# Performance work log

Measured on AMD Instinct MI355X. Metric: run time of the kernel, lower is better.

## Reference

```python
import jax, jax.numpy as jnp
import numpy as np

COMMITMENT_COST = 0.25
N, D, K = 131072, 64, 1024


def setup_inputs() -> dict:
    key = jax.random.key(0)
    k1, k2 = jax.random.split(key)
    inputs = jax.random.normal(k1, (N, D), dtype=jnp.float32)
    # torch init: uniform(-1/K, 1/K)
    weight = jax.random.uniform(k2, (K, D), dtype=jnp.float32,
                                minval=-1.0 / K, maxval=1.0 / K)
    return {"inputs": inputs, "weight": weight}


def reference(inputs, weight):
    x2 = jnp.sum(inputs * inputs, axis=1, keepdims=True)          # [N, 1]
    e2 = jnp.sum(weight * weight, axis=1)                          # [K]
    distances = x2 + e2 - 2.0 * jnp.matmul(inputs, weight.T)       # [N, K]
    encoding_indices = jnp.argmin(distances, axis=1)               # [N]
    # scatter one-hot + matmul in the original == direct gather
    quantized = jnp.take(weight, encoding_indices, axis=0)         # [N, D]
    e_latent_loss = jnp.mean((jax.lax.stop_gradient(quantized) - inputs) ** 2)
    q_latent_loss = jnp.mean((quantized - jax.lax.stop_gradient(inputs)) ** 2)
    loss = q_latent_loss + COMMITMENT_COST * e_latent_loss
    # straight-through estimator
    quantized_st = inputs + jax.lax.stop_gradient(quantized - inputs)
    return (quantized_st, loss, encoding_indices)
```

## Files before the change

kernel.cpp:

```cpp
#include <hip/hip_runtime.h>


#define NROWS 131072
#define DIM 64
#define KCODES 1024
#define MARGIN 5e-5f
#define LOSS_SCALE (1.25f / ((float)NROWS * (float)DIM))

typedef short bf16x8 __attribute__((ext_vector_type(8)));
typedef float f32x4 __attribute__((ext_vector_type(4)));

__device__ __forceinline__ short f2bf(float f) {
    unsigned u = __float_as_uint(f);
    u += 0x7FFF + ((u >> 16) & 1);
    return (short)(u >> 16);
}
__device__ __forceinline__ float bf2f(short h) {
    return __uint_as_float(((unsigned)(unsigned short)h) << 16);
}

__global__ __launch_bounds__(256) void prep_w(const float* __restrict__ w,
                                              float* __restrict__ e2,
                                              short* __restrict__ w_hi,
                                              short* __restrict__ w_lo) {
    int k = blockIdx.x * blockDim.x + threadIdx.x;
    if (k >= KCODES) return;
    const float* wk = w + (size_t)k * DIM;
    float r[DIM];
#pragma unroll
    for (int i = 0; i < DIM / 4; ++i) *(float4*)&r[4 * i] = *(const float4*)(wk + 4 * i);
    float s = 0.f;
#pragma unroll
    for (int d = 0; d < DIM; ++d) s = fmaf(r[d], r[d], s);
    e2[k] = s;

    const int t = k >> 5, ct = (k >> 4) & 1, m = k & 15;
#pragma unroll
    for (int kc = 0; kc < 2; ++kc)
#pragma unroll
        for (int q = 0; q < 4; ++q) {
            bf16x8 hv, lv;
#pragma unroll
            for (int j = 0; j < 8; ++j) {
                float f = r[kc * 32 + q * 8 + j];
                short h = f2bf(f);
                hv[j] = h;
                lv[j] = f2bf(f - bf2f(h));
            }
            size_t fo = ((size_t)(((t * 2 + ct) * 2 + kc) * 4 + q) * 16 + m) * 8;
            *(bf16x8*)(w_hi + fo) = hv;
            *(bf16x8*)(w_lo + fo) = lv;
        }
}

__global__ __launch_bounds__(256, 3) void vq_main(
        const float* __restrict__ x, const float* __restrict__ w,
        const float* __restrict__ e2,
        const short* __restrict__ w_hi, const short* __restrict__ w_lo,
        float* __restrict__ out_q, float* __restrict__ out_loss,
        float* __restrict__ out_idx,
        unsigned* __restrict__ flag_cnt, unsigned* __restrict__ flag_list) {
    const int tid = threadIdx.x;
    const int lane = tid & 63;
    const int wv = tid >> 6;
    const int m = lane & 15;
    const int q = lane >> 4;
    const int block_row0 = blockIdx.x * 128;
    const int wave_row0 = block_row0 + wv * 32;

    __shared__ int sidx[128];
    __shared__ unsigned char sflg[128];
    __shared__ float red[4];

    float xa[2][2][8];
#pragma unroll
    for (int rt = 0; rt < 2; ++rt) {
        const float* xr = x + (size_t)(wave_row0 + rt * 16 + m) * DIM + q * 8;
        *(float4*)&xa[rt][0][0] = *(const float4*)(xr);
        *(float4*)&xa[rt][0][4] = *(const float4*)(xr + 4);
        *(float4*)&xa[rt][1][0] = *(const float4*)(xr + 32);
        *(float4*)&xa[rt][1][4] = *(const float4*)(xr + 36);
    }
    bf16x8 ah[2][2], al[2][2];
#pragma unroll
    for (int rt = 0; rt < 2; ++rt)
#pragma unroll
        for (int c = 0; c < 2; ++c)
#pragma unroll
            for (int j = 0; j < 8; ++j) {
                float f = xa[rt][c][j];
                short h = f2bf(f);
                ah[rt][c][j] = h;
                al[rt][c][j] = f2bf(f - bf2f(h));
            }

    float best[2][4], sec[2][4];
    int bidx[2][4];
#pragma unroll
    for (int rt = 0; rt < 2; ++rt)
#pragma unroll
        for (int r = 0; r < 4; ++r) {
            best[rt][r] = 3.4e38f;
            sec[rt][r] = 3.4e38f;
            bidx[rt][r] = 0;
        }

    const short* ph = w_hi + q * 128 + m * 8;
    const short* pl = w_lo + q * 128 + m * 8;

    for (int t = 0; t < KCODES / 32; ++t) {
        bf16x8 bh[2][2], bl[2][2];
#pragma unroll
        for (int ct = 0; ct < 2; ++ct)
#pragma unroll
            for (int kc = 0; kc < 2; ++kc) {
                int off = t * 2048 + (ct * 2 + kc) * 512;
                bh[ct][kc] = *(const bf16x8*)(ph + off);
                bl[ct][kc] = *(const bf16x8*)(pl + off);
            }
        float e2c0 = e2[t * 32 + m];
        float e2c1 = e2[t * 32 + 16 + m];

        f32x4 acc[2][2];
#pragma unroll
        for (int rt = 0; rt < 2; ++rt)
#pragma unroll
            for (int ct = 0; ct < 2; ++ct) {
                f32x4 a = {0.f, 0.f, 0.f, 0.f};
                a = __builtin_amdgcn_mfma_f32_16x16x32_bf16(al[rt][0], bh[ct][0], a, 0, 0, 0);
                a = __builtin_amdgcn_mfma_f32_16x16x32_bf16(ah[rt][0], bl[ct][0], a, 0, 0, 0);
                a = __builtin_amdgcn_mfma_f32_16x16x32_bf16(ah[rt][0], bh[ct][0], a, 0, 0, 0);
                a = __builtin_amdgcn_mfma_f32_16x16x32_bf16(al[rt][1], bh[ct][1], a, 0, 0, 0);
                a = __builtin_amdgcn_mfma_f32_16x16x32_bf16(ah[rt][1], bl[ct][1], a, 0, 0, 0);
                a = __builtin_amdgcn_mfma_f32_16x16x32_bf16(ah[rt][1], bh[ct][1], a, 0, 0, 0);
                acc[rt][ct] = a;
            }

#pragma unroll
        for (int rt = 0; rt < 2; ++rt)
#pragma unroll
            for (int ct = 0; ct < 2; ++ct) {
                float e2c = ct ? e2c1 : e2c0;
                int id = t * 32 + ct * 16 + m;
#pragma unroll
                for (int r = 0; r < 4; ++r) {
                    float g = fmaf(-2.f, acc[rt][ct][r], e2c);
                    bool c = g < best[rt][r];
                    sec[rt][r] = fminf(sec[rt][r], fmaxf(g, best[rt][r]));
                    if (c) { best[rt][r] = g; bidx[rt][r] = id; }
                }
            }
    }

#pragma unroll
    for (int off = 1; off < 16; off <<= 1)
#pragma unroll
        for (int rt = 0; rt < 2; ++rt)
#pragma unroll
            for (int r = 0; r < 4; ++r) {
                float ob = __shfl_xor(best[rt][r], off, 64);
                int oi = __shfl_xor(bidx[rt][r], off, 64);
                float os = __shfl_xor(sec[rt][r], off, 64);
                float mx = fmaxf(best[rt][r], ob);
                sec[rt][r] = fminf(fminf(sec[rt][r], os), mx);
                bool take = (ob < best[rt][r]) ||
                            (ob == best[rt][r] && oi < bidx[rt][r]);
                if (take) { best[rt][r] = ob; bidx[rt][r] = oi; }
            }

    if (m == 0) {
#pragma unroll
        for (int rt = 0; rt < 2; ++rt)
#pragma unroll
            for (int r = 0; r < 4; ++r) {
                int lr = wv * 32 + rt * 16 + q * 4 + r;
                sidx[lr] = bidx[rt][r];
                bool fl = (sec[rt][r] - best[rt][r]) < MARGIN;
                sflg[lr] = fl ? 1 : 0;
                if (fl) {
                    unsigned p = atomicAdd(flag_cnt, 1u);
                    flag_list[p] = (unsigned)(block_row0 + lr);
                }
            }
    }
    __syncthreads();

    float lsum = 0.f;
    const int rl = tid >> 2, part = tid & 3;
#pragma unroll
    for (int p = 0; p < 2; ++p) {
        int lr = p * 64 + rl;
        int grow = block_row0 + lr;
        if (!sflg[lr]) {
            int bi = sidx[lr];
            const float* xs = x + (size_t)grow * DIM + part * 16;
            const float* ws = w + (size_t)bi * DIM + part * 16;
            float* os = out_q + (size_t)grow * DIM + part * 16;
#pragma unroll
            for (int i = 0; i < 4; ++i) {
                float4 xv = *(const float4*)(xs + 4 * i);
                float4 wv4 = *(const float4*)(ws + 4 * i);
                float d0 = wv4.x - xv.x, d1 = wv4.y - xv.y;
                float d2 = wv4.z - xv.z, d3 = wv4.w - xv.w;
                lsum = fmaf(d0, d0, lsum);
                lsum = fmaf(d1, d1, lsum);
                lsum = fmaf(d2, d2, lsum);
                lsum = fmaf(d3, d3, lsum);
                float4 o = {xv.x + d0, xv.y + d1, xv.z + d2, xv.w + d3};
                *(float4*)(os + 4 * i) = o;
            }
            if (part == 0) out_idx[grow] = (float)bi;
        }
    }

    for (int off = 32; off > 0; off >>= 1) lsum += __shfl_down(lsum, off, 64);
    if ((tid & 63) == 0) red[tid >> 6] = lsum;
    __syncthreads();
    if (tid == 0) {
        float s = (red[0] + red[1]) + (red[2] + red[3]);
        atomicAdd(out_loss, s * LOSS_SCALE);
    }
}

#define CH 16
__global__ __launch_bounds__(256) void vq_cleanup(
        const float* __restrict__ x, const float* __restrict__ w,
        const float* __restrict__ e2,
        const unsigned* __restrict__ flag_cnt,
        const unsigned* __restrict__ flag_list,
        float* __restrict__ out_q, float* __restrict__ out_loss,
        float* __restrict__ out_idx) {
    __shared__ float xs[CH][68];
    __shared__ float wt[128][68];
    __shared__ float sx2[CH];
    const int tid = threadIdx.x;
    const int rowsub = tid >> 4;
    const int kslot = tid & 15;
    const unsigned cnt = *flag_cnt;

    for (unsigned base = blockIdx.x * CH; base < cnt; base += gridDim.x * CH) {
        const int nrows = (int)min((unsigned)CH, cnt - base);
        __syncthreads();
        {
            int rr = tid >> 4, sg = tid & 15;
            if (rr < nrows) {
                unsigned grow = flag_list[base + rr];
                *(float4*)&xs[rr][sg * 4] =
                    *(const float4*)(x + (size_t)grow * DIM + sg * 4);
            }
        }
        __syncthreads();
        if (tid < nrows) {
            float s = 0.f;
#pragma unroll
            for (int d = 0; d < DIM; ++d) s = fmaf(xs[tid][d], xs[tid][d], s);
            sx2[tid] = s;
        }

        unsigned long long kmin = ~0ULL;
        for (int tile = 0; tile < KCODES / 128; ++tile) {
            __syncthreads();
#pragma unroll
            for (int i = 0; i < 8; ++i) {
                int f = tid + i * 256;
                int code = f >> 4, sg = f & 15;
                *(float4*)&wt[code][sg * 4] =
                    *(const float4*)(w + (size_t)(tile * 128 + code) * DIM + sg * 4);
            }
            __syncthreads();
            if (rowsub < nrows) {
#pragma unroll
                for (int j = 0; j < 8; ++j) {
                    int cl = j * 16 + kslot;
                    int code = tile * 128 + cl;
                    float dot = 0.f;
#pragma unroll
                    for (int d4 = 0; d4 < 16; ++d4) {
                        float4 wv4 = *(const float4*)&wt[cl][d4 * 4];
                        float4 xv4 = *(const float4*)&xs[rowsub][d4 * 4];
                        dot = fmaf(wv4.x, xv4.x, dot);
                        dot = fmaf(wv4.y, xv4.y, dot);
                        dot = fmaf(wv4.z, xv4.z, dot);
                        dot = fmaf(wv4.w, xv4.w, dot);
                    }
                    float dist = (sx2[rowsub] + e2[code]) - 2.0f * dot;
                    unsigned long long key =
                        ((unsigned long long)__float_as_uint(dist) << 32) |
                        (unsigned)code;
                    kmin = kmin < key ? kmin : key;
                }
            }
        }
#pragma unroll
        for (int off = 1; off < 16; off <<= 1) {
            unsigned long long o = __shfl_xor(kmin, off, 64);
            kmin = kmin < o ? kmin : o;
        }
        if (rowsub < nrows) {
            int bi = (int)(unsigned)(kmin & 0xFFFFFFFFu);
            unsigned grow = flag_list[base + rowsub];
            float4 x4 = *(float4*)&xs[rowsub][kslot * 4];
            float4 w4 = *(const float4*)(w + (size_t)bi * DIM + kslot * 4);
            float d0 = w4.x - x4.x, d1 = w4.y - x4.y;
            float d2 = w4.z - x4.z, d3 = w4.w - x4.w;
            float ls = 0.f;
            ls = fmaf(d0, d0, ls);
            ls = fmaf(d1, d1, ls);
            ls = fmaf(d2, d2, ls);
            ls = fmaf(d3, d3, ls);
            float4 o = {x4.x + d0, x4.y + d1, x4.z + d2, x4.w + d3};
            *(float4*)(out_q + (size_t)grow * DIM + kslot * 4) = o;
            if (kslot == 0) out_idx[grow] = (float)bi;
#pragma unroll
            for (int off = 1; off < 16; off <<= 1)
                ls += __shfl_xor(ls, off, 64);
            if (kslot == 0) atomicAdd(out_loss, ls * LOSS_SCALE);
        }
    }
}

extern "C" void kernel_launch(void* const* d_in, const int* in_sizes, int n_in,
                              void* d_out, int out_size, void* d_ws, size_t ws_size,
                              hipStream_t stream) {
    const float* x = (const float*)d_in[0];
    const float* w = (const float*)d_in[1];

    float* out_q    = (float*)d_out;
    float* out_loss = (float*)d_out + (size_t)NROWS * DIM;
    float* out_idx  = out_loss + 1;

    float* e2 = (float*)d_ws;
    short* w_hi = (short*)(e2 + KCODES);
    short* w_lo = w_hi + (size_t)KCODES * DIM;
    unsigned* cnt = (unsigned*)(w_lo + (size_t)KCODES * DIM);
    unsigned* list = cnt + 1;

    hipMemsetAsync(out_loss, 0, sizeof(float), stream);
    hipMemsetAsync(cnt, 0, sizeof(unsigned), stream);

    prep_w<<<(KCODES + 255) / 256, 256, 0, stream>>>(w, e2, w_hi, w_lo);
    vq_main<<<NROWS / 128, 256, 0, stream>>>(x, w, e2, w_hi, w_lo,
                                             out_q, out_loss, out_idx, cnt, list);
    vq_cleanup<<<256, 256, 0, stream>>>(x, w, e2, cnt, list,
                                        out_q, out_loss, out_idx);
}
```

Baseline: 209.9 us.

## Double-buffer codebook tile loads, fold -2 scale and e2 into MFMA, drop memsets

Pre-scales the bf16 hi/lo codebook by -2 and seeds the MFMA accumulator with e2, so the per-element fma after the matmul goes away. The main loop is unrolled by two with ping-pong register buffers, so the next tile's loads are issued before the current tile's MFMAs. The two hipMemsetAsync calls are replaced by zeroing inside prep_w, which saves API launches. Costs are extra register pressure from the double buffers, which may hurt occupancy at launch bounds of 3, and slightly different rounding because the -2 scale is applied before the bf16 split.

```diff
diff --git a/kernel.cpp b/kernel.cpp
--- a/kernel.cpp
+++ b/kernel.cpp
@@ -22,8 +22,11 @@
 __global__ __launch_bounds__(256) void prep_w(const float* __restrict__ w,
                                               float* __restrict__ e2,
                                               short* __restrict__ w_hi,
-                                              short* __restrict__ w_lo) {
+                                              short* __restrict__ w_lo,
+                                              float* __restrict__ out_loss,
+                                              unsigned* __restrict__ flag_cnt) {
     int k = blockIdx.x * blockDim.x + threadIdx.x;
+    if (k == 0) { *out_loss = 0.0f; *flag_cnt = 0u; }
     if (k >= KCODES) return;
     const float* wk = w + (size_t)k * DIM;
     float r[DIM];
@@ -42,7 +45,7 @@
             bf16x8 hv, lv;
 #pragma unroll
             for (int j = 0; j < 8; ++j) {
-                float f = r[kc * 32 + q * 8 + j];
+                float f = -2.0f * r[kc * 32 + q * 8 + j];
                 short h = f2bf(f);
                 hv[j] = h;
                 lv[j] = f2bf(f - bf2f(h));
@@ -50,6 +53,35 @@
             size_t fo = ((size_t)(((t * 2 + ct) * 2 + kc) * 4 + q) * 16 + m) * 8;
             *(bf16x8*)(w_hi + fo) = hv;
             *(bf16x8*)(w_lo + fo) = lv;
+        }
+}
+
+__device__ __forceinline__ void compute_tile(
+        int tt, int m,
+        const bf16x8 (&ah)[2][2], const bf16x8 (&al)[2][2],
+        const bf16x8 (&bh)[2][2], const bf16x8 (&bl)[2][2],
+        float ea, float eb,
+        float (&best)[2][4], float (&sec)[2][4], int (&bidx)[2][4]) {
+#pragma unroll
+    for (int rt = 0; rt < 2; ++rt)
+#pragma unroll
+        for (int ct = 0; ct < 2; ++ct) {
+            float ei = ct ? eb : ea;
+            f32x4 a = {ei, ei, ei, ei};
+            a = __builtin_amdgcn_mfma_f32_16x16x32_bf16(al[rt][0], bh[ct][0], a, 0, 0, 0);
+            a = __builtin_amdgcn_mfma_f32_16x16x32_bf16(ah[rt][0], bl[ct][0], a, 0, 0, 0);
+            a = __builtin_amdgcn_mfma_f32_16x16x32_bf16(ah[rt][0], bh[ct][0], a, 0, 0, 0);
+            a = __builtin_amdgcn_mfma_f32_16x16x32_bf16(al[rt][1], bh[ct][1], a, 0, 0, 0);
+            a = __builtin_amdgcn_mfma_f32_16x16x32_bf16(ah[rt][1], bl[ct][1], a, 0, 0, 0);
+            a = __builtin_amdgcn_mfma_f32_16x16x32_bf16(ah[rt][1], bh[ct][1], a, 0, 0, 0);
+            int id = tt * 32 + ct * 16 + m;
+#pragma unroll
+            for (int r = 0; r < 4; ++r) {
+                float g = a[r];
+                bool c = g < best[rt][r];
+                sec[rt][r] = fminf(sec[rt][r], fmaxf(g, best[rt][r]));
+                if (c) { best[rt][r] = g; bidx[rt][r] = id; }
+            }
         }
 }
 
@@ -107,49 +139,51 @@
 
     const short* ph = w_hi + q * 128 + m * 8;
     const short* pl = w_lo + q * 128 + m * 8;
-
-    for (int t = 0; t < KCODES / 32; ++t) {
-        bf16x8 bh[2][2], bl[2][2];
-#pragma unroll
-        for (int ct = 0; ct < 2; ++ct)
-#pragma unroll
-            for (int kc = 0; kc < 2; ++kc) {
-                int off = t * 2048 + (ct * 2 + kc) * 512;
-                bh[ct][kc] = *(const bf16x8*)(ph + off);
-                bl[ct][kc] = *(const bf16x8*)(pl + off);
-            }
-        float e2c0 = e2[t * 32 + m];
-        float e2c1 = e2[t * 32 + 16 + m];
-
-        f32x4 acc[2][2];
-#pragma unroll
-        for (int rt = 0; rt < 2; ++rt)
-#pragma unroll
-            for (int ct = 0; ct < 2; ++ct) {
-                f32x4 a = {0.f, 0.f, 0.f, 0.f};
-                a = __builtin_amdgcn_mfma_f32_16x16x32_bf16(al[rt][0], bh[ct][0], a, 0, 0, 0);
-                a = __builtin_amdgcn_mfma_f32_16x16x32_bf16(ah[rt][0], bl[ct][0], a, 0, 0, 0);
-                a = __builtin_amdgcn_mfma_f32_16x16x32_bf16(ah[rt][0], bh[ct][0], a, 0, 0, 0);
-                a = __builtin_amdgcn_mfma_f32_16x16x32_bf16(al[rt][1], bh[ct][1], a, 0, 0, 0);
-                a = __builtin_amdgcn_mfma_f32_16x16x32_bf16(ah[rt][1], bl[ct][1], a, 0, 0, 0);
-                a = __builtin_amdgcn_mfma_f32_16x16x32_bf16(ah[rt][1], bh[ct][1], a, 0, 0, 0);
-                acc[rt][ct] = a;
-            }
-
-#pragma unroll
-        for (int rt = 0; rt < 2; ++rt)
-#pragma unroll
-            for (int ct = 0; ct < 2; ++ct) {
-                float e2c = ct ? e2c1 : e2c0;
-                int id = t * 32 + ct * 16 + m;
-#pragma unroll
-                for (int r = 0; r < 4; ++r) {
-                    float g = fmaf(-2.f, acc[rt][ct][r], e2c);
-                    bool c = g < best[rt][r];
-                    sec[rt][r] = fminf(sec[rt][r], fmaxf(g, best[rt][r]));
-                    if (c) { best[rt][r] = g; bidx[rt][r] = id; }
+    const float* pe = e2 + m;
+
+    bf16x8 bhA[2][2], blA[2][2], bhB[2][2], blB[2][2];
+    float eaA, ebA, eaB, ebB;
+
+#pragma unroll
+    for (int ct = 0; ct < 2; ++ct)
+#pragma unroll
+        for (int kc = 0; kc < 2; ++kc) {
+            bhA[ct][kc] = *(const bf16x8*)(ph + (ct * 2 + kc) * 512);
+            blA[ct][kc] = *(const bf16x8*)(pl + (ct * 2 + kc) * 512);
+        }
+    eaA = pe[0];
+    ebA = pe[16];
+
+    for (int t = 0; t < KCODES / 32; t += 2) {
+        {
+            const short* p1 = ph + (size_t)(t + 1) * 2048;
+            const short* p2 = pl + (size_t)(t + 1) * 2048;
+#pragma unroll
+            for (int ct = 0; ct < 2; ++ct)
+#pragma unroll
+                for (int kc = 0; kc < 2; ++kc) {
+                    bhB[ct][kc] = *(const bf16x8*)(p1 + (ct * 2 + kc) * 512);
+                    blB[ct][kc] = *(const bf16x8*)(p2 + (ct * 2 + kc) * 512);
                 }
-            }
+            eaB = pe[(t + 1) * 32];
+            ebB = pe[(t + 1) * 32 + 16];
+        }
+        compute_tile(t, m, ah, al, bhA, blA, eaA, ebA, best, sec, bidx);
+        {
+            int tn = (t + 2) & (KCODES / 32 - 1);
+            const short* p1 = ph + (size_t)tn * 2048;
+            const short* p2 = pl + (size_t)tn * 2048;
+#pragma unroll
+            for (int ct = 0; ct < 2; ++ct)
+#pragma unroll
+                for (int kc = 0; kc < 2; ++kc) {
+                    bhA[ct][kc] = *(const bf16x8*)(p1 + (ct * 2 + kc) * 512);
+                    blA[ct][kc] = *(const bf16x8*)(p2 + (ct * 2 + kc) * 512);
+                }
+            eaA = pe[tn * 32];
+            ebA = pe[tn * 32 + 16];
+        }
+        compute_tile(t + 1, m, ah, al, bhB, blB, eaB, ebB, best, sec, bidx);
     }
 
 #pragma unroll
@@ -335,10 +369,8 @@
     unsigned* cnt = (unsigned*)(w_lo + (size_t)KCODES * DIM);
     unsigned* list = cnt + 1;
 
-    hipMemsetAsync(out_loss, 0, sizeof(float), stream);
-    hipMemsetAsync(cnt, 0, sizeof(unsigned), stream);
-
-    prep_w<<<(KCODES + 255) / 256, 256, 0, stream>>>(w, e2, w_hi, w_lo);
+    prep_w<<<(KCODES + 255) / 256, 256, 0, stream>>>(w, e2, w_hi, w_lo,
+                                                     out_loss, cnt);
     vq_main<<<NROWS / 128, 256, 0, stream>>>(x, w, e2, w_hi, w_lo,
                                              out_q, out_loss, out_idx, cnt, list);
     vq_cleanup<<<256, 256, 0, stream>>>(x, w, e2, cnt, list,
```

New measurement: 233.9 us. 1.11x slower.

## Pack code index into distance low bits and fold e2 into MFMA accumulator

Applied to the files above, without the earlier changes.

Pre-scales the codebook by -2 and seeds the MFMA accumulator with |e|^2, so the distance comes straight out of the matrix op without a separate fma. The code index is packed into the low 10 mantissa bits of the distance, so best/second tracking collapses to fminf/fmed3 and the index shuffles and compares disappear. Also removes two memset launches by zeroing the loss and counter inside prep_w, raises the occupancy hint to 4, and doubles the ambiguity margin to offset the truncation precision. The risk is more rows flagged for the exact cleanup pass and occupancy pressure on registers.

```diff
diff --git a/kernel.cpp b/kernel.cpp
--- a/kernel.cpp
+++ b/kernel.cpp
@@ -4,7 +4,7 @@
 #define NROWS 131072
 #define DIM 64
 #define KCODES 1024
-#define MARGIN 5e-5f
+#define MARGIN 1e-4f
 #define LOSS_SCALE (1.25f / ((float)NROWS * (float)DIM))
 
 typedef short bf16x8 __attribute__((ext_vector_type(8)));
@@ -22,8 +22,11 @@
 __global__ __launch_bounds__(256) void prep_w(const float* __restrict__ w,
                                               float* __restrict__ e2,
                                               short* __restrict__ w_hi,
-                                              short* __restrict__ w_lo) {
+                                              short* __restrict__ w_lo,
+                                              float* __restrict__ out_loss,
+                                              unsigned* __restrict__ flag_cnt) {
     int k = blockIdx.x * blockDim.x + threadIdx.x;
+    if (k == 0) { *out_loss = 0.0f; *flag_cnt = 0u; }
     if (k >= KCODES) return;
     const float* wk = w + (size_t)k * DIM;
     float r[DIM];
@@ -42,7 +45,7 @@
             bf16x8 hv, lv;
 #pragma unroll
             for (int j = 0; j < 8; ++j) {
-                float f = r[kc * 32 + q * 8 + j];
+                float f = -2.0f * r[kc * 32 + q * 8 + j];
                 short h = f2bf(f);
                 hv[j] = h;
                 lv[j] = f2bf(f - bf2f(h));
@@ -53,7 +56,7 @@
         }
 }
 
-__global__ __launch_bounds__(256, 3) void vq_main(
+__global__ __launch_bounds__(256, 4) void vq_main(
         const float* __restrict__ x, const float* __restrict__ w,
         const float* __restrict__ e2,
         const short* __restrict__ w_hi, const short* __restrict__ w_lo,
@@ -95,18 +98,17 @@
             }
 
     float best[2][4], sec[2][4];
-    int bidx[2][4];
 #pragma unroll
     for (int rt = 0; rt < 2; ++rt)
 #pragma unroll
         for (int r = 0; r < 4; ++r) {
             best[rt][r] = 3.4e38f;
             sec[rt][r] = 3.4e38f;
-            bidx[rt][r] = 0;
         }
 
     const short* ph = w_hi + q * 128 + m * 8;
     const short* pl = w_lo + q * 128 + m * 8;
+    const float* pe = e2 + m;
 
     for (int t = 0; t < KCODES / 32; ++t) {
         bf16x8 bh[2][2], bl[2][2];
@@ -118,36 +120,28 @@
                 bh[ct][kc] = *(const bf16x8*)(ph + off);
                 bl[ct][kc] = *(const bf16x8*)(pl + off);
             }
-        float e2c0 = e2[t * 32 + m];
-        float e2c1 = e2[t * 32 + 16 + m];
-
-        f32x4 acc[2][2];
+        float e2c0 = pe[t * 32];
+        float e2c1 = pe[t * 32 + 16];
+
 #pragma unroll
         for (int rt = 0; rt < 2; ++rt)
 #pragma unroll
             for (int ct = 0; ct < 2; ++ct) {
-                f32x4 a = {0.f, 0.f, 0.f, 0.f};
+                float ei = ct ? e2c1 : e2c0;
+                f32x4 a = {ei, ei, ei, ei};
                 a = __builtin_amdgcn_mfma_f32_16x16x32_bf16(al[rt][0], bh[ct][0], a, 0, 0, 0);
                 a = __builtin_amdgcn_mfma_f32_16x16x32_bf16(ah[rt][0], bl[ct][0], a, 0, 0, 0);
                 a = __builtin_amdgcn_mfma_f32_16x16x32_bf16(ah[rt][0], bh[ct][0], a, 0, 0, 0);
                 a = __builtin_amdgcn_mfma_f32_16x16x32_bf16(al[rt][1], bh[ct][1], a, 0, 0, 0);
                 a = __builtin_amdgcn_mfma_f32_16x16x32_bf16(ah[rt][1], bl[ct][1], a, 0, 0, 0);
                 a = __builtin_amdgcn_mfma_f32_16x16x32_bf16(ah[rt][1], bh[ct][1], a, 0, 0, 0);
-                acc[rt][ct] = a;
-            }
-
-#pragma unroll
-        for (int rt = 0; rt < 2; ++rt)
-#pragma unroll
-            for (int ct = 0; ct < 2; ++ct) {
-                float e2c = ct ? e2c1 : e2c0;
-                int id = t * 32 + ct * 16 + m;
+                unsigned id = (unsigned)(t * 32 + ct * 16 + m);
 #pragma unroll
                 for (int r = 0; r < 4; ++r) {
-                    float g = fmaf(-2.f, acc[rt][ct][r], e2c);
-                    bool c = g < best[rt][r];
-                    sec[rt][r] = fminf(sec[rt][r], fmaxf(g, best[rt][r]));
-                    if (c) { best[rt][r] = g; bidx[rt][r] = id; }
+                    unsigned kb = (__float_as_uint(a[r]) & 0xFFFFFC00u) | id;
+                    float kf = __uint_as_float(kb);
+                    sec[rt][r] = __builtin_amdgcn_fmed3f(kf, best[rt][r], sec[rt][r]);
+                    best[rt][r] = fminf(best[rt][r], kf);
                 }
             }
     }
@@ -159,13 +153,9 @@
 #pragma unroll
             for (int r = 0; r < 4; ++r) {
                 float ob = __shfl_xor(best[rt][r], off, 64);
-                int oi = __shfl_xor(bidx[rt][r], off, 64);
                 float os = __shfl_xor(sec[rt][r], off, 64);
-                float mx = fmaxf(best[rt][r], ob);
-                sec[rt][r] = fminf(fminf(sec[rt][r], os), mx);
-                bool take = (ob < best[rt][r]) ||
-                            (ob == best[rt][r] && oi < bidx[rt][r]);
-                if (take) { best[rt][r] = ob; bidx[rt][r] = oi; }
+                sec[rt][r] = fminf(fminf(sec[rt][r], os), fmaxf(best[rt][r], ob));
+                best[rt][r] = fminf(best[rt][r], ob);
             }
 
     if (m == 0) {
@@ -173,9 +163,13 @@
         for (int rt = 0; rt < 2; ++rt)
 #pragma unroll
             for (int r = 0; r < 4; ++r) {
+                unsigned bb = __float_as_uint(best[rt][r]);
+                int code = (int)(bb & 1023u);
+                float bestm = __uint_as_float(bb & 0xFFFFFC00u);
+                float secm = __uint_as_float(__float_as_uint(sec[rt][r]) & 0xFFFFFC00u);
                 int lr = wv * 32 + rt * 16 + q * 4 + r;
-                sidx[lr] = bidx[rt][r];
-                bool fl = (sec[rt][r] - best[rt][r]) < MARGIN;
+                sidx[lr] = code;
+                bool fl = (secm - bestm) < MARGIN;
                 sflg[lr] = fl ? 1 : 0;
                 if (fl) {
                     unsigned p = atomicAdd(flag_cnt, 1u);
@@ -335,10 +329,8 @@
     unsigned* cnt = (unsigned*)(w_lo + (size_t)KCODES * DIM);
     unsigned* list = cnt + 1;
 
-    hipMemsetAsync(out_loss, 0, sizeof(float), stream);
-    hipMemsetAsync(cnt, 0, sizeof(unsigned), stream);
-
-    prep_w<<<(KCODES + 255) / 256, 256, 0, stream>>>(w, e2, w_hi, w_lo);
+    prep_w<<<(KCODES + 255) / 256, 256, 0, stream>>>(w, e2, w_hi, w_lo,
+                                                     out_loss, cnt);
     vq_main<<<NROWS / 128, 256, 0, stream>>>(x, w, e2, w_hi, w_lo,
                                              out_q, out_loss, out_idx, cnt, list);
     vq_cleanup<<<256, 256, 0, stream>>>(x, w, e2, cnt, list,
```

New measurement: 261.8 us. 24.8% more time.

## Double-buffer codebook tiles in LDS via async global-to-LDS loads

Applied to the files above, without the earlier changes.

Codebook hi/lo bf16 tiles are now staged into a double-buffered LDS array with global_load_lds, prefetching the next tile while the current one is consumed, with a barrier each iteration. The -2 factor is folded into the prepared weights and e2 seeds the MFMA accumulator, which drops the per-element fma. The two memsets are folded into prep_w, and occupancy is raised to 4 blocks per SM. This costs an extra __syncthreads per tile and adds register pressure under the tighter launch bound. Any code in the unseen remainder (e.g. vq_cleanup's margin check) that assumed unscaled w_hi/w_lo or the old distance form may now be affected.

```diff
diff --git a/kernel.cpp b/kernel.cpp
--- a/kernel.cpp
+++ b/kernel.cpp
@@ -19,11 +19,20 @@
     return __uint_as_float(((unsigned)(unsigned short)h) << 16);
 }
 
+__device__ __forceinline__ void gload_lds16(const short* g, short* l) {
+    __builtin_amdgcn_global_load_lds(
+        (const __attribute__((address_space(1))) void*)g,
+        (__attribute__((address_space(3))) void*)l, 16, 0, 0);
+}
+
 __global__ __launch_bounds__(256) void prep_w(const float* __restrict__ w,
                                               float* __restrict__ e2,
                                               short* __restrict__ w_hi,
-                                              short* __restrict__ w_lo) {
+                                              short* __restrict__ w_lo,
+                                              float* __restrict__ out_loss,
+                                              unsigned* __restrict__ flag_cnt) {
     int k = blockIdx.x * blockDim.x + threadIdx.x;
+    if (k == 0) { *out_loss = 0.0f; *flag_cnt = 0u; }
     if (k >= KCODES) return;
     const float* wk = w + (size_t)k * DIM;
     float r[DIM];
@@ -42,7 +51,7 @@
             bf16x8 hv, lv;
 #pragma unroll
             for (int j = 0; j < 8; ++j) {
-                float f = r[kc * 32 + q * 8 + j];
+                float f = -2.0f * r[kc * 32 + q * 8 + j];
                 short h = f2bf(f);
                 hv[j] = h;
                 lv[j] = f2bf(f - bf2f(h));
@@ -53,7 +62,7 @@
         }
 }
 
-__global__ __launch_bounds__(256, 3) void vq_main(
+__global__ __launch_bounds__(256, 4) void vq_main(
         const float* __restrict__ x, const float* __restrict__ w,
         const float* __restrict__ e2,
         const short* __restrict__ w_hi, const short* __restrict__ w_lo,
@@ -68,9 +77,17 @@
     const int block_row0 = blockIdx.x * 128;
     const int wave_row0 = block_row0 + wv * 32;
 
+    __shared__ short lds_b[2][4096];
     __shared__ int sidx[128];
     __shared__ unsigned char sflg[128];
     __shared__ float red[4];
+
+    {
+        const short* gh = w_hi + wv * 512 + lane * 8;
+        const short* gl = w_lo + wv * 512 + lane * 8;
+        gload_lds16(gh, &lds_b[0][wv * 512]);
+        gload_lds16(gl, &lds_b[0][2048 + wv * 512]);
+    }
 
     float xa[2][2][8];
 #pragma unroll
@@ -105,51 +122,56 @@
             bidx[rt][r] = 0;
         }
 
-    const short* ph = w_hi + q * 128 + m * 8;
-    const short* pl = w_lo + q * 128 + m * 8;
+    float e2a = e2[m], e2b = e2[16 + m];
+    __syncthreads();
 
     for (int t = 0; t < KCODES / 32; ++t) {
+        const int cur = t & 1;
+        if (t < KCODES / 32 - 1) {
+            const short* gh = w_hi + (size_t)(t + 1) * 2048 + wv * 512 + lane * 8;
+            const short* gl = w_lo + (size_t)(t + 1) * 2048 + wv * 512 + lane * 8;
+            gload_lds16(gh, &lds_b[cur ^ 1][wv * 512]);
+            gload_lds16(gl, &lds_b[cur ^ 1][2048 + wv * 512]);
+        }
+        const int tn = (t + 1) & (KCODES / 32 - 1);
+        float e2an = e2[tn * 32 + m];
+        float e2bn = e2[tn * 32 + 16 + m];
+
         bf16x8 bh[2][2], bl[2][2];
 #pragma unroll
         for (int ct = 0; ct < 2; ++ct)
 #pragma unroll
             for (int kc = 0; kc < 2; ++kc) {
-                int off = t * 2048 + (ct * 2 + kc) * 512;
-                bh[ct][kc] = *(const bf16x8*)(ph + off);
-                bl[ct][kc] = *(const bf16x8*)(pl + off);
-            }
-        float e2c0 = e2[t * 32 + m];
-        float e2c1 = e2[t * 32 + 16 + m];
-
-        f32x4 acc[2][2];
+                int off = (ct * 2 + kc) * 512 + lane * 8;
+                bh[ct][kc] = *(const bf16x8*)&lds_b[cur][off];
+                bl[ct][kc] = *(const bf16x8*)&lds_b[cur][2048 + off];
+            }
+
 #pragma unroll
         for (int rt = 0; rt < 2; ++rt)
 #pragma unroll
             for (int ct = 0; ct < 2; ++ct) {
-                f32x4 a = {0.f, 0.f, 0.f, 0.f};
+                float ei = ct ? e2b : e2a;
+                f32x4 a = {ei, ei, ei, ei};
                 a = __builtin_amdgcn_mfma_f32_16x16x32_bf16(al[rt][0], bh[ct][0], a, 0, 0, 0);
                 a = __builtin_amdgcn_mfma_f32_16x16x32_bf16(ah[rt][0], bl[ct][0], a, 0, 0, 0);
                 a = __builtin_amdgcn_mfma_f32_16x16x32_bf16(ah[rt][0], bh[ct][0], a, 0, 0, 0);
                 a = __builtin_amdgcn_mfma_f32_16x16x32_bf16(al[rt][1], bh[ct][1], a, 0, 0, 0);
                 a = __builtin_amdgcn_mfma_f32_16x16x32_bf16(ah[rt][1], bl[ct][1], a, 0, 0, 0);
                 a = __builtin_amdgcn_mfma_f32_16x16x32_bf16(ah[rt][1], bh[ct][1], a, 0, 0, 0);
-                acc[rt][ct] = a;
-            }
-
-#pragma unroll
-        for (int rt = 0; rt < 2; ++rt)
-#pragma unroll
-            for (int ct = 0; ct < 2; ++ct) {
-                float e2c = ct ? e2c1 : e2c0;
                 int id = t * 32 + ct * 16 + m;
 #pragma unroll
                 for (int r = 0; r < 4; ++r) {
-                    float g = fmaf(-2.f, acc[rt][ct][r], e2c);
+                    float g = a[r];
                     bool c = g < best[rt][r];
                     sec[rt][r] = fminf(sec[rt][r], fmaxf(g, best[rt][r]));
                     if (c) { best[rt][r] = g; bidx[rt][r] = id; }
                 }
             }
+
+        __syncthreads();
+        e2a = e2an;
+        e2b = e2bn;
     }
 
 #pragma unroll
@@ -335,10 +357,8 @@
     unsigned* cnt = (unsigned*)(w_lo + (size_t)KCODES * DIM);
     unsigned* list = cnt + 1;
 
-    hipMemsetAsync(out_loss, 0, sizeof(float), stream);
-    hipMemsetAsync(cnt, 0, sizeof(unsigned), stream);
-
-    prep_w<<<(KCODES + 255) / 256, 256, 0, stream>>>(w, e2, w_hi, w_lo);
+    prep_w<<<(KCODES + 255) / 256, 256, 0, stream>>>(w, e2, w_hi, w_lo,
+                                                     out_loss, cnt);
     vq_main<<<NROWS / 128, 256, 0, stream>>>(x, w, e2, w_hi, w_lo,
                                              out_q, out_loss, out_idx, cnt, list);
     vq_cleanup<<<256, 256, 0, stream>>>(x, w, e2, cnt, list,
```

New measurement: 211.6 us. About the same (+0.8%).
